# Kernel optimization log

Hardware: AMD Instinct MI355X
Metric: run time of the kernel (lower is better)

## Reference

```python
import jax, jax.numpy as jnp
import numpy as np

N = 100000      # nodes
E = 1600000     # edges
F_IN = 512      # input features
H = 64          # hidden
R = 2           # relations
B = 30          # bases
NEG_SLOPE = 0.2 # GATConv default


def setup_inputs() -> dict:
    key = jax.random.key(0)
    ks = jax.random.split(key, 14)
    s_in = 1.0 / np.sqrt(F_IN)
    s_h = 1.0 / np.sqrt(H)
    return {
        "x": jax.random.normal(ks[0], (N, F_IN), jnp.float32),
        "edge_index": jax.random.randint(ks[1], (2, E), 0, N),
        "edge_types": jax.random.randint(ks[2], (E,), 0, R),
        # RGCN layer 1 (F_IN -> H), basis-decomposed
        "basis1": jax.random.normal(ks[3], (B, F_IN, H), jnp.float32) * s_in,
        "comp1": jax.random.normal(ks[4], (R, B), jnp.float32) * (1.0 / np.sqrt(B)),
        "root1": jax.random.normal(ks[5], (F_IN, H), jnp.float32) * s_in,
        "bias1": jnp.zeros((H,), jnp.float32),
        # RGCN layer 2 (H -> H)
        "basis2": jax.random.normal(ks[6], (B, H, H), jnp.float32) * s_h,
        "comp2": jax.random.normal(ks[7], (R, B), jnp.float32) * (1.0 / np.sqrt(B)),
        "root2": jax.random.normal(ks[8], (H, H), jnp.float32) * s_h,
        "bias2": jnp.zeros((H,), jnp.float32),
        # GAT (H -> 1, heads=1)
        "gat_w": jax.random.normal(ks[9], (H, 1), jnp.float32) * s_h,
        "att_src": jax.random.normal(ks[10], (1,), jnp.float32),
        "att_dst": jax.random.normal(ks[11], (1,), jnp.float32),
        "gat_bias": jnp.zeros((1,), jnp.float32),
    }


def rgcn_layer(x, src, dst, etype, basis, comp, root, bias):
    # W_r = sum_b comp[r,b] * basis[b]; transform nodes once per relation,
    # then gather per edge (math-equal to PyG's per-edge transform, cheaper).
    W = jnp.einsum('rb,bio->rio', comp, basis)       # [R, in, out]
    h = jnp.einsum('ni,rio->rno', x, W)              # [R, N, out]
    out = x @ root + bias                            # root/self term
    for r in range(R):                               # R=2, fixed small loop
        m = (etype == r).astype(x.dtype)             # [E]
        msg = h[r][src] * m[:, None]                 # gather + mask
        agg = jax.ops.segment_sum(msg, dst, num_segments=N)
        cnt = jax.ops.segment_sum(m, dst, num_segments=N)
        out = out + agg / jnp.maximum(cnt, 1.0)[:, None]   # mean aggr per relation
    return out


def gat_layer(x, src, dst, gat_w, att_src, att_dst, gat_bias):
    # GATConv with heads=1, out=1, add_self_loops=True, negative_slope=0.2
    loop = jnp.arange(N)
    s = jnp.concatenate([src, loop])
    d = jnp.concatenate([dst, loop])
    h = x @ gat_w                                    # [N, 1]
    a_s = h[:, 0] * att_src[0]                       # [N]
    a_d = h[:, 0] * att_dst[0]                       # [N]
    e = jax.nn.leaky_relu(a_s[s] + a_d[d], NEG_SLOPE)  # [E+N]
    emax = jax.ops.segment_max(e, d, num_segments=N)   # every dst has self-loop
    ex = jnp.exp(e - emax[d])
    denom = jax.ops.segment_sum(ex, d, num_segments=N)
    alpha = ex / denom[d]                            # segment softmax over dst
    out = jax.ops.segment_sum(alpha[:, None] * h[s], d, num_segments=N)
    return out + gat_bias


def reference(x, edge_index, edge_types,
              basis1, comp1, root1, bias1,
              basis2, comp2, root2, bias2,
              gat_w, att_src, att_dst, gat_bias):
    src, dst = edge_index[0], edge_index[1]
    x1 = jax.nn.relu(rgcn_layer(x, src, dst, edge_types, basis1, comp1, root1, bias1))
    x2 = rgcn_layer(x1, src, dst, edge_types, basis2, comp2, root2, bias2)
    return gat_layer(x2, src, dst, gat_w, att_src, att_dst, gat_bias)  # [N, 1]
```

## Files before the change

kernel.cpp:

```cpp
#include <hip/hip_runtime.h>
#include <hip/hip_bf16.h>
#include <math.h>

#define NCOL 192
#define BB   30
#define SCAN_T 256
#define SCAN_ELEMS 1024

typedef short bf16x8 __attribute__((ext_vector_type(8)));
typedef float f32x4  __attribute__((ext_vector_type(4)));
typedef unsigned short u16x8 __attribute__((ext_vector_type(8)));

__device__ __forceinline__ ushort f2bf(float f) {
  unsigned u = __float_as_uint(f);
  unsigned r = u + 0x7fff + ((u >> 16) & 1);
  return (ushort)(r >> 16);
}
__device__ __forceinline__ float bf2f(ushort u) {
  return __uint_as_float(((unsigned)u) << 16);
}

__global__ void hist_deg(const int* __restrict__ dst, int* __restrict__ deg, int E) {
  int e = blockIdx.x * blockDim.x + threadIdx.x;
  if (e >= E) return;
  atomicAdd(&deg[dst[e]], 1);
}

__global__ __launch_bounds__(SCAN_T) void scan_local(const int* __restrict__ deg,
                                                     int* __restrict__ rowptr,
                                                     int* __restrict__ partial, int N) {
  __shared__ int sdata[SCAN_T];
  int t = threadIdx.x;
  int base = blockIdx.x * SCAN_ELEMS + t * 4;
  int v[4], s = 0;
#pragma unroll
  for (int k = 0; k < 4; ++k) {
    v[k] = (base + k < N) ? deg[base + k] : 0;
    s += v[k];
  }
  sdata[t] = s;
  __syncthreads();
  for (int off = 1; off < SCAN_T; off <<= 1) {
    int add = (t >= off) ? sdata[t - off] : 0;
    __syncthreads();
    sdata[t] += add;
    __syncthreads();
  }
  int run = sdata[t] - s;
  if (t == SCAN_T - 1) partial[blockIdx.x] = sdata[t];
#pragma unroll
  for (int k = 0; k < 4; ++k) {
    if (base + k <= N) rowptr[base + k] = run;
    run += v[k];
  }
}

__global__ __launch_bounds__(SCAN_T) void scan_partial(int* __restrict__ partial, int nb) {
  __shared__ int sdata[SCAN_T];
  int t = threadIdx.x;
  int v = (t < nb) ? partial[t] : 0;
  sdata[t] = v;
  __syncthreads();
  for (int off = 1; off < SCAN_T; off <<= 1) {
    int add = (t >= off) ? sdata[t - off] : 0;
    __syncthreads();
    sdata[t] += add;
    __syncthreads();
  }
  if (t < nb) partial[t] = sdata[t] - v;
  if (t == nb - 1) partial[nb] = sdata[t];
}

__global__ void scatter_edges(const int* __restrict__ src, const int* __restrict__ dst,
                              const int* __restrict__ et, const int* __restrict__ rowptr,
                              const int* __restrict__ partial,
                              int* __restrict__ fill, int* __restrict__ srcpk, int E) {
  int e = blockIdx.x * blockDim.x + threadIdx.x;
  if (e >= E) return;
  int d = dst[e];
  int pos = rowptr[d] + partial[d >> 10] + atomicAdd(&fill[d], 1);
  srcpk[pos] = src[e] | (et[e] << 30);
}

__device__ __forceinline__ void wpk_one(const float* __restrict__ basis,
                                        const float* __restrict__ comp,
                                        const float* __restrict__ root,
                                        ushort* __restrict__ Wpk, int Kin, int idx) {
  int k = idx / NCOL, j = idx - k * NCOL;
  float v;
  if (j < 64) {
    v = root[k * 64 + j];
  } else {
    int r = (j >> 6) - 1, o = j & 63;
    float s = 0.f;
#pragma unroll
    for (int b = 0; b < BB; ++b)
      s = fmaf(comp[r * BB + b], basis[((size_t)b * Kin + k) * 64 + o], s);
    v = s;
  }
  int chunk = k >> 6, kg = (k >> 3) & 7, elem = k & 7;
  int slot = (kg * NCOL + j) ^ kg;
  Wpk[(size_t)chunk * 12288 + slot * 8 + elem] = f2bf(v);
}

__global__ void build_wpk_both(const float* __restrict__ basis1, const float* __restrict__ comp1,
                               const float* __restrict__ root1,
                               const float* __restrict__ basis2, const float* __restrict__ comp2,
                               const float* __restrict__ root2,
                               ushort* __restrict__ Wpk1, ushort* __restrict__ Wpk2) {
  int idx = blockIdx.x * blockDim.x + threadIdx.x;
  if (idx < 512 * NCOL) {
    wpk_one(basis1, comp1, root1, Wpk1, 512, idx);
  } else {
    idx -= 512 * NCOL;
    if (idx < 64 * NCOL) wpk_one(basis2, comp2, root2, Wpk2, 64, idx);
  }
}

template <int K, int BF16IN>
__global__ __launch_bounds__(256, 3) void gemm_mfma(const void* __restrict__ Xv,
                                                    const ushort* __restrict__ Wpk,
                                                    ushort* __restrict__ Y, int N) {
  constexpr int NC = K / 64;
  constexpr int NB = (NC > 1) ? 2 : 1;
  __shared__ ushort Ws[NB * 12288];

  const int tid  = threadIdx.x;
  const int wid  = tid >> 6;
  const int lane = tid & 63;
  const int lrow = lane & 15;
  const int lhi  = lane >> 4;
  const int row0 = blockIdx.x * 64 + wid * 16;

  int lr = row0 + lrow;
  if (lr >= N) lr = N - 1;
  const float*  Xf = (const float*)Xv  + (size_t)lr * K;
  const ushort* Xh = (const ushort*)Xv + (size_t)lr * K;

  const ushort* wsrc = Wpk + wid * 3072 + lane * 8;
  u16x8 wr[6];
#define LOAD_W(c)                                                             \
  { _Pragma("unroll") for (int i = 0; i < 6; ++i)                             \
      wr[i] = *(const u16x8*)(wsrc + (size_t)(c) * 12288 + i * 512); }
#define WRITE_W(buf)                                                          \
  { ushort* dst = Ws + (buf) * 12288 + wid * 3072 + lane * 8;                 \
    _Pragma("unroll") for (int i = 0; i < 6; ++i)                             \
      *(u16x8*)(dst + i * 512) = wr[i]; }

  float4 pa[2][4];
  u16x8  ph[2][2];
#define LOAD_A(c, slot)                                                       \
  if constexpr (BF16IN) {                                                     \
    ph[slot][0] = ((const u16x8*)Xh)[(c) * 8 + lhi];                          \
    ph[slot][1] = ((const u16x8*)Xh)[(c) * 8 + 4 + lhi];                      \
  } else {                                                                    \
    _Pragma("unroll") for (int q = 0; q < 4; ++q)                             \
      pa[slot][q] = ((const float4*)Xf)[(c) * 16 + (q >> 1) * 8 + lhi * 2 + (q & 1)]; \
  }
#define MAT_A(slot, tt, areg)                                                 \
  if constexpr (BF16IN) {                                                     \
    areg = (bf16x8)ph[slot][tt];                                              \
  } else {                                                                    \
    float4 v0 = pa[slot][(tt) * 2], v1 = pa[slot][(tt) * 2 + 1];              \
    areg[0] = (short)f2bf(v0.x); areg[1] = (short)f2bf(v0.y);                 \
    areg[2] = (short)f2bf(v0.z); areg[3] = (short)f2bf(v0.w);                 \
    areg[4] = (short)f2bf(v1.x); areg[5] = (short)f2bf(v1.y);                 \
    areg[6] = (short)f2bf(v1.z); areg[7] = (short)f2bf(v1.w);                 \
  }
#define COMP(buf, tt, areg)                                                   \
  { const int kg = (tt) * 4 + lhi;                                            \
    const ushort* ls = Ws + (buf) * 12288;                                    \
    _Pragma("unroll") for (int h = 0; h < 2; ++h) {                           \
      bf16x8 b[6];                                                            \
      _Pragma("unroll") for (int q = 0; q < 6; ++q) {                         \
        int slot = (kg * NCOL + (h * 6 + q) * 16 + lrow) ^ (kg & 7);          \
        b[q] = *(const bf16x8*)(ls + slot * 8);                               \
      }                                                                       \
      _Pragma("unroll") for (int q = 0; q < 6; ++q)                           \
        acc[h * 6 + q] = __builtin_amdgcn_mfma_f32_16x16x32_bf16(areg, b[q],  \
                                                     acc[h * 6 + q], 0, 0, 0); \
    } }

  LOAD_W(0)
  LOAD_A(0, 0)
  if constexpr (NC > 1) { LOAD_A(1, 1) }
  WRITE_W(0)
  __syncthreads();

  f32x4 acc[12];
#pragma unroll
  for (int cc = 0; cc < 12; ++cc) acc[cc] = (f32x4){0.f, 0.f, 0.f, 0.f};

#pragma unroll
  for (int c = 0; c < NC; ++c) {
    bf16x8 a0, a1;
    MAT_A(c & 1, 0, a0)
    MAT_A(c & 1, 1, a1)
    if (c + 2 < NC) { LOAD_A(c + 2, c & 1) }
    if (c + 1 < NC) { LOAD_W(c + 1) }
    COMP(NB > 1 ? (c & 1) : 0, 0, a0)
    COMP(NB > 1 ? (c & 1) : 0, 1, a1)
    if (c + 1 < NC) {
      WRITE_W((c + 1) & 1)
      __syncthreads();
    }
  }
#undef LOAD_W
#undef WRITE_W
#undef LOAD_A
#undef MAT_A
#undef COMP

#pragma unroll
  for (int cc = 0; cc < 12; ++cc) {
#pragma unroll
    for (int j = 0; j < 4; ++j) {
      int r = row0 + lhi * 4 + j;
      if (r < N) Y[(size_t)r * NCOL + cc * 16 + lrow] = f2bf(acc[cc][j]);
    }
  }
}

template <int RELU, int GATH>
__global__ __launch_bounds__(256) void fused_agg(const ushort* __restrict__ Y,
                                                 const int* __restrict__ rowptr,
                                                 const int* __restrict__ partial,
                                                 const int* __restrict__ srcpk,
                                                 const float* __restrict__ bias,
                                                 const float* __restrict__ gw,
                                                 ushort* __restrict__ accout,
                                                 float* __restrict__ hval, int N) {
  int n = blockIdx.x * 4 + (threadIdx.x >> 6);
  if (n >= N) return;
  const int lane = threadIdx.x & 63;
  const int g    = lane >> 3;
  const int f0   = (lane & 7) * 8;

  float a0[8], a1[8];
#pragma unroll
  for (int j = 0; j < 8; ++j) { a0[j] = 0.f; a1[j] = 0.f; }
  float c0 = 0.f, c1 = 0.f;

  const int beg = rowptr[n] + partial[n >> 10];
  const int end = rowptr[n + 1] + partial[(n + 1) >> 10];
  for (int i = beg; i < end; i += 16) {
    int eA = i + g, eB = i + 8 + g;
    bool vA = eA < end, vB = eB < end;
    int pkA = 0, pkB = 0;
    if (vA) pkA = srcpk[eA];
    if (vB) pkB = srcpk[eB];
    u16x8 xA = (u16x8){0, 0, 0, 0, 0, 0, 0, 0}, xB = xA;
    if (vA) xA = *(const u16x8*)(Y + (size_t)(pkA & 0x3fffffff) * NCOL + 64 +
                                 ((pkA >> 30) << 6) + f0);
    if (vB) xB = *(const u16x8*)(Y + (size_t)(pkB & 0x3fffffff) * NCOL + 64 +
                                 ((pkB >> 30) << 6) + f0);
    float rA = (vA && (pkA >> 30)) ? 1.f : 0.f;
    float sA = vA ? 1.f : 0.f;
    float rB = (vB && (pkB >> 30)) ? 1.f : 0.f;
    float sB = vB ? 1.f : 0.f;
    c0 += (sA - rA) + (sB - rB);
    c1 += rA + rB;
#pragma unroll
    for (int j = 0; j < 8; ++j) {
      float fA = bf2f(xA[j]), fB = bf2f(xB[j]);
      a0[j] += (sA - rA) * fA + (sB - rB) * fB;
      a1[j] += rA * fA + rB * fB;
    }
  }

#pragma unroll
  for (int msk = 8; msk <= 32; msk <<= 1) {
#pragma unroll
    for (int j = 0; j < 8; ++j) {
      a0[j] += __shfl_xor(a0[j], msk);
      a1[j] += __shfl_xor(a1[j], msk);
    }
    c0 += __shfl_xor(c0, msk);
    c1 += __shfl_xor(c1, msk);
  }

  float inv0 = 1.f / fmaxf(c0, 1.f);
  float inv1 = 1.f / fmaxf(c1, 1.f);
  u16x8 rv = *(const u16x8*)(Y + (size_t)n * NCOL + f0);
  float4 bA = *(const float4*)(bias + f0);
  float4 bB = *(const float4*)(bias + f0 + 4);
  float bb[8] = {bA.x, bA.y, bA.z, bA.w, bB.x, bB.y, bB.z, bB.w};
  float res[8];
#pragma unroll
  for (int j = 0; j < 8; ++j) {
    float v = bf2f(rv[j]) + bb[j] + a0[j] * inv0 + a1[j] * inv1;
    res[j] = RELU ? fmaxf(v, 0.f) : v;
  }
  if (accout && g == 0) {
    u16x8 o;
#pragma unroll
    for (int j = 0; j < 8; ++j) o[j] = f2bf(res[j]);
    *(u16x8*)(accout + (size_t)n * 64 + f0) = o;
  }
  if (GATH) {
    float4 gA = *(const float4*)(gw + f0);
    float4 gB = *(const float4*)(gw + f0 + 4);
    float gg[8] = {gA.x, gA.y, gA.z, gA.w, gB.x, gB.y, gB.z, gB.w};
    float dot = 0.f;
#pragma unroll
    for (int j = 0; j < 8; ++j) dot = fmaf(res[j], gg[j], dot);
    dot += __shfl_xor(dot, 1);
    dot += __shfl_xor(dot, 2);
    dot += __shfl_xor(dot, 4);
    if (lane == 0) hval[n] = dot;
  }
}

__device__ __forceinline__ float leaky(float x) { return x > 0.f ? x : 0.2f * x; }

__global__ __launch_bounds__(256) void gat_csr(const int* __restrict__ rowptr,
                                               const int* __restrict__ partial,
                                               const int* __restrict__ srcpk,
                                               const float* __restrict__ hval,
                                               const float* __restrict__ as_,
                                               const float* __restrict__ ad_,
                                               const float* __restrict__ gb,
                                               float* __restrict__ out, int N) {
  int n = blockIdx.x * 4 + (threadIdx.x >> 6);
  if (n >= N) return;
  const int lane = threadIdx.x & 63;
  float as = *as_, ad = *ad_;
  float hv = hval[n];
  float adn = hv * ad;
  float eself = leaky(hv * as + adn);
  const int beg = rowptr[n] + partial[n >> 10];
  const int end = rowptr[n + 1] + partial[(n + 1) >> 10];
  int deg = end - beg;
  float m, den, acc;
  if (deg <= 64) {
    bool valid = lane < deg;
    float hs = 0.f;
    if (valid) hs = hval[srcpk[beg + lane] & 0x3fffffff];
    float e = valid ? leaky(hs * as + adn) : -3.4e38f;
    m = fmaxf(e, eself);
#pragma unroll
    for (int o = 32; o > 0; o >>= 1) m = fmaxf(m, __shfl_xor(m, o));
    float ex = valid ? expf(e - m) : 0.f;
    den = ex;
    acc = ex * hs;
#pragma unroll
    for (int o = 32; o > 0; o >>= 1) {
      den += __shfl_xor(den, o);
      acc += __shfl_xor(acc, o);
    }
  } else {
    m = eself;
    for (int i = beg + lane; i < end; i += 64)
      m = fmaxf(m, leaky(hval[srcpk[i] & 0x3fffffff] * as + adn));
#pragma unroll
    for (int o = 32; o > 0; o >>= 1) m = fmaxf(m, __shfl_xor(m, o));
    float dl = 0.f, al = 0.f;
    for (int i = beg + lane; i < end; i += 64) {
      float hs = hval[srcpk[i] & 0x3fffffff];
      float ex = expf(leaky(hs * as + adn) - m);
      dl += ex;
      al += ex * hs;
    }
    den = dl;
    acc = al;
#pragma unroll
    for (int o = 32; o > 0; o >>= 1) {
      den += __shfl_xor(den, o);
      acc += __shfl_xor(acc, o);
    }
  }
  float es = expf(eself - m);
  den += es;
  acc += es * hv;
  if (lane == 0) out[n] = acc / den + *gb;
}

extern "C" void kernel_launch(void* const* d_in, const int* in_sizes, int n_in,
                              void* d_out, int out_size, void* d_ws, size_t ws_size,
                              hipStream_t stream) {
  const float* x      = (const float*)d_in[0];
  const int*   eidx   = (const int*)d_in[1];
  const int*   etype  = (const int*)d_in[2];
  const float* basis1 = (const float*)d_in[3];
  const float* comp1  = (const float*)d_in[4];
  const float* root1  = (const float*)d_in[5];
  const float* bias1  = (const float*)d_in[6];
  const float* basis2 = (const float*)d_in[7];
  const float* comp2  = (const float*)d_in[8];
  const float* root2  = (const float*)d_in[9];
  const float* bias2  = (const float*)d_in[10];
  const float* gat_w  = (const float*)d_in[11];
  const float* att_s  = (const float*)d_in[12];
  const float* att_d  = (const float*)d_in[13];
  const float* gat_b  = (const float*)d_in[14];

  const int N = in_sizes[0] / 512;
  const int E = in_sizes[1] / 2;
  const int* src = eidx;
  const int* dst = eidx + E;

  char* p = (char*)d_ws;
  ushort* Y    = (ushort*)p; p += (size_t)N * NCOL * 2;
  ushort* acc1 = (ushort*)p; p += (size_t)N * 64 * 2;
  ushort* Wpk1 = (ushort*)p; p += (size_t)512 * NCOL * 2;
  ushort* Wpk2 = (ushort*)p; p += (size_t)64 * NCOL * 2;
  float* hval  = (float*)p;  p += (size_t)N * 4;
  int* deg     = (int*)p;    p += (size_t)N * 4;
  int* fill    = (int*)p;    p += (size_t)N * 4;
  int* rowptr  = (int*)p;    p += (size_t)(N + 16) * 4;
  int* partial = (int*)p;    p += (size_t)(SCAN_T + 16) * 4;
  int* srcpk   = (int*)p;    p += (size_t)E * 4;
  float* out   = (float*)d_out;

  const int TB = 256;
  const int GB = (N + 63) / 64;
  const int nb = (N + 1 + SCAN_ELEMS - 1) / SCAN_ELEMS;

  hipMemsetAsync(deg, 0, (size_t)2 * N * sizeof(int), stream);
  hist_deg<<<(E + TB - 1) / TB, TB, 0, stream>>>(dst, deg, E);
  scan_local<<<nb, SCAN_T, 0, stream>>>(deg, rowptr, partial, N);
  scan_partial<<<1, SCAN_T, 0, stream>>>(partial, nb);
  scatter_edges<<<(E + TB - 1) / TB, TB, 0, stream>>>(src, dst, etype, rowptr, partial,
                                                      fill, srcpk, E);

  build_wpk_both<<<(576 * NCOL + TB - 1) / TB, TB, 0, stream>>>(basis1, comp1, root1,
                                                                basis2, comp2, root2,
                                                                Wpk1, Wpk2);

  gemm_mfma<512, 0><<<GB, 256, 0, stream>>>(x, Wpk1, Y, N);
  fused_agg<1, 0><<<(N + 3) / 4, TB, 0, stream>>>(Y, rowptr, partial, srcpk, bias1, nullptr,
                                                  acc1, nullptr, N);

  gemm_mfma<64, 1><<<GB, 256, 0, stream>>>(acc1, Wpk2, Y, N);
  fused_agg<0, 1><<<(N + 3) / 4, TB, 0, stream>>>(Y, rowptr, partial, srcpk, bias2, gat_w,
                                                  nullptr, hval, N);

  gat_csr<<<(N + 3) / 4, TB, 0, stream>>>(rowptr, partial, srcpk, hval, att_s, att_d, gat_b,
                                          out, N);
}
```

Before: 392.1 us.

## Fold layer-2 weights and GAT projection into vectors, drop second GEMM

Because layer 2 has no activation and feeds straight into the GAT linear projection, the layer-2 weight matrices (root and per-relation) are pre-multiplied by gat_w into three 64-vectors plus a bias scalar. The second aggregation then gathers the 64-wide h1 rows and computes hval with dot products, which removes the second MFMA GEMM and its 192-column intermediate writes and reads. The gather loop is also unrolled to four edges per lane group, and the memset is replaced by a zeroing kernel. Precomputing the weights this way changes the floating-point summation order.

```diff
diff --git a/kernel.cpp b/kernel.cpp
--- a/kernel.cpp
+++ b/kernel.cpp
@@ -18,6 +18,11 @@
 }
 __device__ __forceinline__ float bf2f(ushort u) {
   return __uint_as_float(((unsigned)u) << 16);
+}
+
+__global__ void zero_int(int* __restrict__ p, int n) {
+  int i = blockIdx.x * blockDim.x + threadIdx.x;
+  if (i < n) p[i] = 0;
 }
 
 __global__ void hist_deg(const int* __restrict__ dst, int* __restrict__ deg, int E) {
@@ -82,38 +87,51 @@
   srcpk[pos] = src[e] | (et[e] << 30);
 }
 
-__device__ __forceinline__ void wpk_one(const float* __restrict__ basis,
-                                        const float* __restrict__ comp,
-                                        const float* __restrict__ root,
-                                        ushort* __restrict__ Wpk, int Kin, int idx) {
-  int k = idx / NCOL, j = idx - k * NCOL;
-  float v;
-  if (j < 64) {
-    v = root[k * 64 + j];
-  } else {
-    int r = (j >> 6) - 1, o = j & 63;
-    float s = 0.f;
-#pragma unroll
-    for (int b = 0; b < BB; ++b)
-      s = fmaf(comp[r * BB + b], basis[((size_t)b * Kin + k) * 64 + o], s);
-    v = s;
-  }
-  int chunk = k >> 6, kg = (k >> 3) & 7, elem = k & 7;
-  int slot = (kg * NCOL + j) ^ kg;
-  Wpk[(size_t)chunk * 12288 + slot * 8 + elem] = f2bf(v);
-}
-
-__global__ void build_wpk_both(const float* __restrict__ basis1, const float* __restrict__ comp1,
-                               const float* __restrict__ root1,
-                               const float* __restrict__ basis2, const float* __restrict__ comp2,
-                               const float* __restrict__ root2,
-                               ushort* __restrict__ Wpk1, ushort* __restrict__ Wpk2) {
+__global__ void build_weights(const float* __restrict__ basis1, const float* __restrict__ comp1,
+                              const float* __restrict__ root1,
+                              const float* __restrict__ basis2, const float* __restrict__ comp2,
+                              const float* __restrict__ root2,
+                              const float* __restrict__ bias2, const float* __restrict__ gw,
+                              ushort* __restrict__ Wpk1, float* __restrict__ w2g,
+                              float* __restrict__ cb) {
   int idx = blockIdx.x * blockDim.x + threadIdx.x;
   if (idx < 512 * NCOL) {
-    wpk_one(basis1, comp1, root1, Wpk1, 512, idx);
-  } else {
-    idx -= 512 * NCOL;
-    if (idx < 64 * NCOL) wpk_one(basis2, comp2, root2, Wpk2, 64, idx);
+    int k = idx / NCOL, j = idx - k * NCOL;
+    float v;
+    if (j < 64) {
+      v = root1[k * 64 + j];
+    } else {
+      int r = (j >> 6) - 1, o = j & 63;
+      float s = 0.f;
+#pragma unroll
+      for (int b = 0; b < BB; ++b)
+        s = fmaf(comp1[r * BB + b], basis1[((size_t)b * 512 + k) * 64 + o], s);
+      v = s;
+    }
+    int chunk = k >> 6, kg = (k >> 3) & 7, elem = k & 7;
+    int slot = (kg * NCOL + j) ^ kg;
+    Wpk1[(size_t)chunk * 12288 + slot * 8 + elem] = f2bf(v);
+    return;
+  }
+  int c = idx - 512 * NCOL;
+  if (c < 192) {
+    int k = c & 63, part = c >> 6;
+    float s = 0.f;
+    if (part == 0) {
+      for (int o = 0; o < 64; ++o) s = fmaf(root2[k * 64 + o], gw[o], s);
+    } else {
+      int r = part - 1;
+      for (int b = 0; b < BB; ++b) {
+        float bs = 0.f;
+        for (int o = 0; o < 64; ++o) bs = fmaf(basis2[((size_t)b * 64 + k) * 64 + o], gw[o], bs);
+        s = fmaf(comp2[r * BB + b], bs, s);
+      }
+    }
+    w2g[c] = s;
+  } else if (c == 192) {
+    float s = 0.f;
+    for (int o = 0; o < 64; ++o) s = fmaf(bias2[o], gw[o], s);
+    *cb = s;
   }
 }
 
@@ -221,15 +239,12 @@
   }
 }
 
-template <int RELU, int GATH>
-__global__ __launch_bounds__(256) void fused_agg(const ushort* __restrict__ Y,
-                                                 const int* __restrict__ rowptr,
-                                                 const int* __restrict__ partial,
-                                                 const int* __restrict__ srcpk,
-                                                 const float* __restrict__ bias,
-                                                 const float* __restrict__ gw,
-                                                 ushort* __restrict__ accout,
-                                                 float* __restrict__ hval, int N) {
+__global__ __launch_bounds__(256) void agg_layer1(const ushort* __restrict__ Y,
+                                                  const int* __restrict__ rowptr,
+                                                  const int* __restrict__ partial,
+                                                  const int* __restrict__ srcpk,
+                                                  const float* __restrict__ bias,
+                                                  ushort* __restrict__ h1, int N) {
   int n = blockIdx.x * 4 + (threadIdx.x >> 6);
   if (n >= N) return;
   const int lane = threadIdx.x & 63;
@@ -243,28 +258,33 @@
 
   const int beg = rowptr[n] + partial[n >> 10];
   const int end = rowptr[n + 1] + partial[(n + 1) >> 10];
-  for (int i = beg; i < end; i += 16) {
-    int eA = i + g, eB = i + 8 + g;
-    bool vA = eA < end, vB = eB < end;
-    int pkA = 0, pkB = 0;
-    if (vA) pkA = srcpk[eA];
-    if (vB) pkB = srcpk[eB];
-    u16x8 xA = (u16x8){0, 0, 0, 0, 0, 0, 0, 0}, xB = xA;
-    if (vA) xA = *(const u16x8*)(Y + (size_t)(pkA & 0x3fffffff) * NCOL + 64 +
-                                 ((pkA >> 30) << 6) + f0);
-    if (vB) xB = *(const u16x8*)(Y + (size_t)(pkB & 0x3fffffff) * NCOL + 64 +
-                                 ((pkB >> 30) << 6) + f0);
-    float rA = (vA && (pkA >> 30)) ? 1.f : 0.f;
-    float sA = vA ? 1.f : 0.f;
-    float rB = (vB && (pkB >> 30)) ? 1.f : 0.f;
-    float sB = vB ? 1.f : 0.f;
-    c0 += (sA - rA) + (sB - rB);
-    c1 += rA + rB;
-#pragma unroll
-    for (int j = 0; j < 8; ++j) {
-      float fA = bf2f(xA[j]), fB = bf2f(xB[j]);
-      a0[j] += (sA - rA) * fA + (sB - rB) * fB;
-      a1[j] += rA * fA + rB * fB;
+  for (int i = beg; i < end; i += 32) {
+    int pk[4]; bool vv[4];
+    u16x8 xv[4];
+#pragma unroll
+    for (int u = 0; u < 4; ++u) {
+      int e = i + u * 8 + g;
+      vv[u] = e < end;
+      pk[u] = vv[u] ? srcpk[e] : 0;
+    }
+#pragma unroll
+    for (int u = 0; u < 4; ++u) {
+      xv[u] = (u16x8){0, 0, 0, 0, 0, 0, 0, 0};
+      if (vv[u]) xv[u] = *(const u16x8*)(Y + (size_t)(pk[u] & 0x3fffffff) * NCOL + 64 +
+                                         ((pk[u] >> 30) << 6) + f0);
+    }
+#pragma unroll
+    for (int u = 0; u < 4; ++u) {
+      float r = (vv[u] && (pk[u] >> 30)) ? 1.f : 0.f;
+      float s = vv[u] ? 1.f : 0.f;
+      c0 += s - r;
+      c1 += r;
+#pragma unroll
+      for (int j = 0; j < 8; ++j) {
+        float f = bf2f(xv[u][j]);
+        a0[j] = fmaf(s - r, f, a0[j]);
+        a1[j] = fmaf(r, f, a1[j]);
+      }
     }
   }
 
@@ -279,36 +299,106 @@
     c1 += __shfl_xor(c1, msk);
   }
 
+  if (g == 0) {
+    float inv0 = 1.f / fmaxf(c0, 1.f);
+    float inv1 = 1.f / fmaxf(c1, 1.f);
+    u16x8 rv = *(const u16x8*)(Y + (size_t)n * NCOL + f0);
+    float4 bA = *(const float4*)(bias + f0);
+    float4 bB = *(const float4*)(bias + f0 + 4);
+    float bb[8] = {bA.x, bA.y, bA.z, bA.w, bB.x, bB.y, bB.z, bB.w};
+    u16x8 o;
+#pragma unroll
+    for (int j = 0; j < 8; ++j) {
+      float v = bf2f(rv[j]) + bb[j] + a0[j] * inv0 + a1[j] * inv1;
+      o[j] = f2bf(fmaxf(v, 0.f));
+    }
+    *(u16x8*)(h1 + (size_t)n * 64 + f0) = o;
+  }
+}
+
+__global__ __launch_bounds__(256) void agg_layer2(const ushort* __restrict__ h1,
+                                                  const int* __restrict__ rowptr,
+                                                  const int* __restrict__ partial,
+                                                  const int* __restrict__ srcpk,
+                                                  const float* __restrict__ w2g,
+                                                  const float* __restrict__ cb,
+                                                  float* __restrict__ hval, int N) {
+  int n = blockIdx.x * 4 + (threadIdx.x >> 6);
+  if (n >= N) return;
+  const int lane = threadIdx.x & 63;
+  const int g    = lane >> 3;
+  const int f0   = (lane & 7) * 8;
+
+  float a0[8], a1[8];
+#pragma unroll
+  for (int j = 0; j < 8; ++j) { a0[j] = 0.f; a1[j] = 0.f; }
+  float c0 = 0.f, c1 = 0.f;
+
+  const int beg = rowptr[n] + partial[n >> 10];
+  const int end = rowptr[n + 1] + partial[(n + 1) >> 10];
+  for (int i = beg; i < end; i += 32) {
+    int pk[4]; bool vv[4];
+    u16x8 xv[4];
+#pragma unroll
+    for (int u = 0; u < 4; ++u) {
+      int e = i + u * 8 + g;
+      vv[u] = e < end;
+      pk[u] = vv[u] ? srcpk[e] : 0;
+    }
+#pragma unroll
+    for (int u = 0; u < 4; ++u) {
+      xv[u] = (u16x8){0, 0, 0, 0, 0, 0, 0, 0};
+      if (vv[u]) xv[u] = *(const u16x8*)(h1 + (size_t)(pk[u] & 0x3fffffff) * 64 + f0);
+    }
+#pragma unroll
+    for (int u = 0; u < 4; ++u) {
+      float r = (vv[u] && (pk[u] >> 30)) ? 1.f : 0.f;
+      float s = vv[u] ? 1.f : 0.f;
+      c0 += s - r;
+      c1 += r;
+#pragma unroll
+      for (int j = 0; j < 8; ++j) {
+        float f = bf2f(xv[u][j]);
+        a0[j] = fmaf(s - r, f, a0[j]);
+        a1[j] = fmaf(r, f, a1[j]);
+      }
+    }
+  }
+
+#pragma unroll
+  for (int msk = 8; msk <= 32; msk <<= 1) {
+#pragma unroll
+    for (int j = 0; j < 8; ++j) {
+      a0[j] += __shfl_xor(a0[j], msk);
+      a1[j] += __shfl_xor(a1[j], msk);
+    }
+    c0 += __shfl_xor(c0, msk);
+    c1 += __shfl_xor(c1, msk);
+  }
+
   float inv0 = 1.f / fmaxf(c0, 1.f);
   float inv1 = 1.f / fmaxf(c1, 1.f);
-  u16x8 rv = *(const u16x8*)(Y + (size_t)n * NCOL + f0);
-  float4 bA = *(const float4*)(bias + f0);
-  float4 bB = *(const float4*)(bias + f0 + 4);
-  float bb[8] = {bA.x, bA.y, bA.z, bA.w, bB.x, bB.y, bB.z, bB.w};
-  float res[8];
+  u16x8 hv = *(const u16x8*)(h1 + (size_t)n * 64 + f0);
+  float4 wA = *(const float4*)(w2g + f0);
+  float4 wB = *(const float4*)(w2g + f0 + 4);
+  float4 uA = *(const float4*)(w2g + 64 + f0);
+  float4 uB = *(const float4*)(w2g + 64 + f0 + 4);
+  float4 vA = *(const float4*)(w2g + 128 + f0);
+  float4 vB = *(const float4*)(w2g + 128 + f0 + 4);
+  float wv[8] = {wA.x, wA.y, wA.z, wA.w, wB.x, wB.y, wB.z, wB.w};
+  float uv[8] = {uA.x, uA.y, uA.z, uA.w, uB.x, uB.y, uB.z, uB.w};
+  float vv8[8] = {vA.x, vA.y, vA.z, vA.w, vB.x, vB.y, vB.z, vB.w};
+  float dot = 0.f;
 #pragma unroll
   for (int j = 0; j < 8; ++j) {
-    float v = bf2f(rv[j]) + bb[j] + a0[j] * inv0 + a1[j] * inv1;
-    res[j] = RELU ? fmaxf(v, 0.f) : v;
-  }
-  if (accout && g == 0) {
-    u16x8 o;
-#pragma unroll
-    for (int j = 0; j < 8; ++j) o[j] = f2bf(res[j]);
-    *(u16x8*)(accout + (size_t)n * 64 + f0) = o;
-  }
-  if (GATH) {
-    float4 gA = *(const float4*)(gw + f0);
-    float4 gB = *(const float4*)(gw + f0 + 4);
-    float gg[8] = {gA.x, gA.y, gA.z, gA.w, gB.x, gB.y, gB.z, gB.w};
-    float dot = 0.f;
-#pragma unroll
-    for (int j = 0; j < 8; ++j) dot = fmaf(res[j], gg[j], dot);
-    dot += __shfl_xor(dot, 1);
-    dot += __shfl_xor(dot, 2);
-    dot += __shfl_xor(dot, 4);
-    if (lane == 0) hval[n] = dot;
-  }
+    dot = fmaf(bf2f(hv[j]), wv[j], dot);
+    dot = fmaf(a0[j] * inv0, uv[j], dot);
+    dot = fmaf(a1[j] * inv1, vv8[j], dot);
+  }
+  dot += __shfl_xor(dot, 1);
+  dot += __shfl_xor(dot, 2);
+  dot += __shfl_xor(dot, 4);
+  if (lane == 0) hval[n] = dot + *cb;
 }
 
 __device__ __forceinline__ float leaky(float x) { return x > 0.f ? x : 0.2f * x; }
@@ -401,9 +491,10 @@
 
   char* p = (char*)d_ws;
   ushort* Y    = (ushort*)p; p += (size_t)N * NCOL * 2;
-  ushort* acc1 = (ushort*)p; p += (size_t)N * 64 * 2;
+  ushort* h1   = (ushort*)p; p += (size_t)N * 64 * 2;
   ushort* Wpk1 = (ushort*)p; p += (size_t)512 * NCOL * 2;
-  ushort* Wpk2 = (ushort*)p; p += (size_t)64 * NCOL * 2;
+  float* w2g   = (float*)p;  p += 192 * 4;
+  float* cb    = (float*)p;  p += 16 * 4;
   float* hval  = (float*)p;  p += (size_t)N * 4;
   int* deg     = (int*)p;    p += (size_t)N * 4;
   int* fill    = (int*)p;    p += (size_t)N * 4;
@@ -416,24 +507,20 @@
   const int GB = (N + 63) / 64;
   const int nb = (N + 1 + SCAN_ELEMS - 1) / SCAN_ELEMS;
 
-  hipMemsetAsync(deg, 0, (size_t)2 * N * sizeof(int), stream);
+  zero_int<<<(2 * N + TB - 1) / TB, TB, 0, stream>>>(deg, 2 * N);
   hist_deg<<<(E + TB - 1) / TB, TB, 0, stream>>>(dst, deg, E);
   scan_local<<<nb, SCAN_T, 0, stream>>>(deg, rowptr, partial, N);
   scan_partial<<<1, SCAN_T, 0, stream>>>(partial, nb);
   scatter_edges<<<(E + TB - 1) / TB, TB, 0, stream>>>(src, dst, etype, rowptr, partial,
                                                       fill, srcpk, E);
 
-  build_wpk_both<<<(576 * NCOL + TB - 1) / TB, TB, 0, stream>>>(basis1, comp1, root1,
-                                                                basis2, comp2, root2,
-                                                                Wpk1, Wpk2);
+  build_weights<<<(512 * NCOL + 256 + TB - 1) / TB, TB, 0, stream>>>(
+      basis1, comp1, root1, basis2, comp2, root2, bias2, gat_w, Wpk1, w2g, cb);
 
   gemm_mfma<512, 0><<<GB, 256, 0, stream>>>(x, Wpk1, Y, N);
-  fused_agg<1, 0><<<(N + 3) / 4, TB, 0, stream>>>(Y, rowptr, partial, srcpk, bias1, nullptr,
-                                                  acc1, nullptr, N);
-
-  gemm_mfma<64, 1><<<GB, 256, 0, stream>>>(acc1, Wpk2, Y, N);
-  fused_agg<0, 1><<<(N + 3) / 4, TB, 0, stream>>>(Y, rowptr, partial, srcpk, bias2, gat_w,
-                                                  nullptr, hval, N);
+  agg_layer1<<<(N + 3) / 4, TB, 0, stream>>>(Y, rowptr, partial, srcpk, bias1, h1, N);
+
+  agg_layer2<<<(N + 3) / 4, TB, 0, stream>>>(h1, rowptr, partial, srcpk, w2g, cb, hval, N);
 
   gat_csr<<<(N + 3) / 4, TB, 0, stream>>>(rowptr, partial, srcpk, hval, att_s, att_d, gat_b,
                                           out, N);
```

New measurement: 427.3 us. 1.09x slower.
